# Kernel optimization log

Hardware: AMD Instinct MI355X
Metric: run time of the kernel (lower is better)

The kernel has to match this reference:

```python
import jax, jax.numpy as jnp
import numpy as np

D_MODEL = 1024
H = 16          # n_heads (kv heads)
G = 2           # n_gqa_groups
DQ = 64         # d_queries
DV = 64         # d_values
MAXLEN = 2048
NSEG = 8
SEG = MAXLEN // NSEG  # 256
EPS = 1e-5
ROPE_THETA = 10000.0


def setup_inputs() -> dict:
    key = jax.random.key(0)
    ks = jax.random.split(key, 10)
    N = 8
    w = lambda k, sh: jax.random.normal(k, sh, dtype=jnp.float32) * 0.02
    return {
        "query_sequences": jax.random.normal(ks[0], (N, MAXLEN, D_MODEL), dtype=jnp.float32),
        "key_sequences": jax.random.normal(ks[1], (N, MAXLEN, D_MODEL), dtype=jnp.float32),
        "value_sequences": jax.random.normal(ks[2], (N, MAXLEN, D_MODEL), dtype=jnp.float32),
        "ln_w": jnp.ones((D_MODEL,), dtype=jnp.float32),
        "ln_b": jnp.zeros((D_MODEL,), dtype=jnp.float32),
        "Wq": w(ks[3], (G * H * DQ, D_MODEL)),
        "Wk": w(ks[4], (H * DQ, D_MODEL)),
        "Wv": w(ks[5], (H * DV, D_MODEL)),
        "Wo": w(ks[6], (D_MODEL, H * DV)),
        "Wkc": w(ks[7], (DQ, SEG * DQ)),
        "bkc": jnp.zeros((DQ,), dtype=jnp.float32),
        "Wvc": w(ks[8], (DV, SEG * DV)),
        "bvc": jnp.zeros((DV,), dtype=jnp.float32),
    }


def _layernorm(x, w, b):
    mu = x.mean(-1, keepdims=True)
    var = ((x - mu) ** 2).mean(-1, keepdims=True)
    return (x - mu) * jax.lax.rsqrt(var + EPS) * w + b


def _rope(x):
    # x: [..., seq, DQ]; full-dim interleaved RoPE (rotary-embedding-torch convention)
    seq = x.shape[-2]
    inv_freq = 1.0 / (ROPE_THETA ** (jnp.arange(0, DQ, 2, dtype=jnp.float32) / DQ))  # [DQ/2]
    ang = jnp.arange(seq, dtype=jnp.float32)[:, None] * inv_freq[None, :]            # [seq, DQ/2]
    ang = jnp.repeat(ang, 2, axis=-1)                                                # [seq, DQ]
    cos, sin = jnp.cos(ang), jnp.sin(ang)
    x2 = x.reshape(x.shape[:-1] + (DQ // 2, 2))
    xrot = jnp.stack([-x2[..., 1], x2[..., 0]], axis=-1).reshape(x.shape)
    return x * cos + xrot * sin


def _forward(query_sequences, key_sequences, value_sequences,
             ln_w, ln_b, Wq, Wk, Wv, Wo, Wkc, bkc, Wvc, bvc):
    N, t, _ = query_sequences.shape
    q = _layernorm(query_sequences, ln_w, ln_b)
    k = _layernorm(key_sequences, ln_w, ln_b)
    v = _layernorm(value_sequences, ln_w, ln_b)

    qh = (q @ Wq.T).reshape(N, t, G, H, DQ).transpose(0, 2, 3, 1, 4)  # [N,G,H,t,DQ]
    kh = (k @ Wk.T).reshape(N, t, H, DQ).transpose(0, 2, 1, 3)        # [N,H,T,DQ]
    vh = (v @ Wv.T).reshape(N, t, H, DV).transpose(0, 2, 1, 3)        # [N,H,T,DV]

    qh = _rope(qh)
    kh = _rope(kh)

    # split into NSEG segments along time; keep last 2 raw, compress the rest
    kseg = kh.reshape(N, H, NSEG, SEG, DQ)
    vseg = vh.reshape(N, H, NSEG, SEG, DV)
    recent_k = kseg[:, :, -2:].reshape(N, H, 2 * SEG, DQ)
    recent_v = vseg[:, :, -2:].reshape(N, H, 2 * SEG, DV)
    k_sum = jax.nn.elu(kseg[:, :, :-2].reshape(N, H, NSEG - 2, SEG * DQ) @ Wkc.T + bkc)  # [N,H,S-2,DQ]
    v_sum = jax.nn.elu(vseg[:, :, :-2].reshape(N, H, NSEG - 2, SEG * DV) @ Wvc.T + bvc)
    K = jnp.concatenate([k_sum, recent_k], axis=-2)  # [N,H,Tk,DQ], Tk = (NSEG-2) + 2*SEG
    V = jnp.concatenate([v_sum, recent_v], axis=-2)

    # NOTE: original einsum sums over the GQA group axis g
    attn = jnp.einsum('nghtq,nhTq->nhtT', qh, K) * (1.0 / DQ ** 0.5)
    attn = 30.0 * jnp.tanh(attn / 30.0)  # grok scaled attn

    Tk = K.shape[-2]
    causal = jnp.arange(Tk)[None, :] <= jnp.arange(t)[:, None]  # tril slice [t, Tk]
    attn = jnp.where(causal, attn, -jnp.inf)
    attn = jax.nn.softmax(attn, axis=-1)

    out = jnp.einsum('nhtT,nhTv->nhtv', attn, V)
    out = out.transpose(0, 2, 1, 3).reshape(N, t, H * DV)
    return out @ Wo.T


def reference(query_sequences, key_sequences, value_sequences,
              ln_w, ln_b, Wq, Wk, Wv, Wo, Wkc, bkc, Wvc, bvc):
    return _forward(query_sequences, key_sequences, value_sequences,
                    ln_w, ln_b, Wq, Wk, Wv, Wo, Wkc, bkc, Wvc, bvc)
```

## Files before the change

### kernel.cpp

```cpp
#include <hip/hip_runtime.h>
#include <stdint.h>

#define DEV static __device__ __forceinline__

typedef unsigned short u16;
typedef unsigned int u32;
typedef __attribute__((ext_vector_type(4))) float f32x4;
typedef __attribute__((ext_vector_type(8))) short bf16x8;

DEV float bf2f(u16 u) { u32 x = ((u32)u) << 16; float f; __builtin_memcpy(&f, &x, 4); return f; }
DEV u16 f2bf(float f) { u32 x; __builtin_memcpy(&x, &f, 4); x = x + 0x7fffu + ((x >> 16) & 1u); return (u16)(x >> 16); }
DEV float lo16(u32 p) { u32 x = p << 16; float f; __builtin_memcpy(&f, &x, 4); return f; }
DEV float hi16(u32 p) { u32 x = p & 0xffff0000u; float f; __builtin_memcpy(&f, &x, 4); return f; }
DEV u32 pack2(float a, float b) { return (u32)f2bf(a) | ((u32)f2bf(b) << 16); }

DEV u32 cvtpk(float lo, float hi) {
  u32 r; asm("v_cvt_pk_bf16_f32 %0, %1, %2" : "=v"(r) : "v"(lo), "v"(hi)); return r;
}
DEV bf16x8 pk8(f32x4 a, f32x4 b) {
  union { u32 u[4]; bf16x8 v; } x;
  x.u[0] = cvtpk(a[0], a[1]); x.u[1] = cvtpk(a[2], a[3]);
  x.u[2] = cvtpk(b[0], b[1]); x.u[3] = cvtpk(b[2], b[3]);
  return x.v;
}

DEV f32x4 mfma16(bf16x8 a, bf16x8 b, f32x4 c) {
  return __builtin_amdgcn_mfma_f32_16x16x32_bf16(a, b, c, 0, 0, 0);
}

DEV void gl_lds16(const u16* g, u16* l) {
  __builtin_amdgcn_global_load_lds((const __attribute__((address_space(1))) void*)g,
                                   (__attribute__((address_space(3))) void*)l, 16, 0, 0);
}

__global__ __launch_bounds__(256) void prep_all_kernel(
    const float* __restrict__ Wq, const float* __restrict__ Wk, const float* __restrict__ Wv,
    const float* __restrict__ Wo, const float* __restrict__ Wkc, const float* __restrict__ Wvc,
    u16* __restrict__ wqe, u16* __restrict__ wkb, u16* __restrict__ wvb,
    u16* __restrict__ wob, u16* __restrict__ wkcb, u16* __restrict__ wvcb,
    float* __restrict__ cs) {
  int b = blockIdx.x;
  if (b < 6144) {
    int which = b >> 10;
    int id = (b & 1023) * 256 + threadIdx.x;
    const float* src; u16* dst;
    switch (which) {
      case 0: src = Wq;  dst = wqe;  break;
      case 1: src = Wk;  dst = wkb;  break;
      case 2: src = Wv;  dst = wvb;  break;
      case 3: src = Wo;  dst = wob;  break;
      case 4: src = Wkc; dst = wkcb; break;
      default: src = Wvc; dst = wvcb; break;
    }
    float4 a = ((const float4*)src)[id];
    if (which == 0) {
      float4 c = ((const float4*)Wq)[id + 262144];
      a.x += c.x; a.y += c.y; a.z += c.z; a.w += c.w;
    }
    ushort4 o; o.x = f2bf(a.x); o.y = f2bf(a.y); o.z = f2bf(a.z); o.w = f2bf(a.w);
    ((ushort4*)dst)[id] = o;
  } else {
    int id = (b - 6144) * 256 + threadIdx.x;
    int t = id >> 5, i = id & 31;
    double ang = (double)t * pow(10000.0, -(double)(2 * i) / 64.0);
    cs[id * 2] = (float)cos(ang);
    cs[id * 2 + 1] = (float)sin(ang);
  }
}

__global__ __launch_bounds__(256) void ln_kernel(const float* __restrict__ x, const float* __restrict__ w,
                                                 const float* __restrict__ b, u16* __restrict__ out) {
  int row = blockIdx.x, t = threadIdx.x;
  float4 v = ((const float4*)(x + (size_t)row * 1024))[t];
  float s = v.x + v.y + v.z + v.w;
  float s2 = v.x * v.x + v.y * v.y + v.z * v.z + v.w * v.w;
#pragma unroll
  for (int off = 32; off; off >>= 1) { s += __shfl_xor(s, off, 64); s2 += __shfl_xor(s2, off, 64); }
  __shared__ float red[8];
  if ((t & 63) == 0) { red[t >> 6] = s; red[4 + (t >> 6)] = s2; }
  __syncthreads();
  s = red[0] + red[1] + red[2] + red[3];
  s2 = red[4] + red[5] + red[6] + red[7];
  float mu = s * 0.0009765625f;
  float var = s2 * 0.0009765625f - mu * mu;
  float rstd = rsqrtf(var + 1e-5f);
  float4 wv = ((const float4*)w)[t];
  float4 bv = ((const float4*)b)[t];
  ushort4 o;
  o.x = f2bf((v.x - mu) * rstd * wv.x + bv.x);
  o.y = f2bf((v.y - mu) * rstd * wv.y + bv.y);
  o.z = f2bf((v.z - mu) * rstd * wv.z + bv.z);
  o.w = f2bf((v.w - mu) * rstd * wv.w + bv.w);
  *(ushort4*)(out + (size_t)row * 1024 + t * 4) = o;
}

template <int MODE>
__global__ __launch_bounds__(512, 4) void gemm_nt(const u16* __restrict__ A, const u16* __restrict__ B,
                                                  void* __restrict__ Cout, int M, int Nd, int K,
                                                  const float* __restrict__ cs) {
  __shared__ u16 As[16384], Bs[8192];
  int tid = threadIdx.x, lane = tid & 63, wv = tid >> 6;
  int l15 = lane & 15, lq = lane >> 4;
  int bm = blockIdx.x * 256, bn = blockIdx.y * 128;
  int wm = (wv >> 1) * 64, wn = (wv & 1) * 64;
  int srow_in = lane >> 3, sslot = lane & 7;
  f32x4 acc[4][4] = {};
  for (int k0 = 0; k0 < K; k0 += 64) {
    __syncthreads();
#pragma unroll
    for (int it = 0; it < 4; ++it) {
      int ia = it * 8 + wv;
      int row = ia * 8 + srow_in;
      int gc = sslot ^ (row & 7);
      gl_lds16(A + (size_t)(bm + row) * K + k0 + gc * 8, &As[ia * 512]);
    }
#pragma unroll
    for (int it = 0; it < 2; ++it) {
      int ia = it * 8 + wv;
      int row = ia * 8 + srow_in;
      int gc = sslot ^ (row & 7);
      gl_lds16(B + (size_t)(bn + row) * K + k0 + gc * 8, &Bs[ia * 512]);
    }
    __syncthreads();
#pragma unroll
    for (int h = 0; h < 2; ++h) {
      bf16x8 af[4], bfr[4];
#pragma unroll
      for (int mt = 0; mt < 4; ++mt) {
        int r = wm + mt * 16 + l15;
        af[mt] = *(const bf16x8*)&As[r * 64 + (((h * 4 + lq) ^ (r & 7)) * 8)];
      }
#pragma unroll
      for (int nt = 0; nt < 4; ++nt) {
        int r = wn + nt * 16 + l15;
        bfr[nt] = *(const bf16x8*)&Bs[r * 64 + (((h * 4 + lq) ^ (r & 7)) * 8)];
      }
#pragma unroll
      for (int mt = 0; mt < 4; ++mt)
#pragma unroll
        for (int nt = 0; nt < 4; ++nt)
          acc[mt][nt] = mfma16(af[mt], bfr[nt], acc[mt][nt]);
    }
  }
#pragma unroll
  for (int mt = 0; mt < 4; ++mt)
#pragma unroll
    for (int nt = 0; nt < 4; ++nt)
#pragma unroll
      for (int i = 0; i < 4; ++i) {
        int row = bm + wm + mt * 16 + lq * 4 + i;
        int col = bn + wn + nt * 16 + l15;
        float x = acc[mt][nt][i];
        if (MODE == 1) {
          ((float*)Cout)[(size_t)row * Nd + col] = x;
        } else if (MODE == 0) {
          ((u16*)Cout)[(size_t)row * Nd + col] = f2bf(x);
        } else {
          float xp = __shfl_xor(x, 1, 64);
          int t = row & 2047;
          int i0 = (col & 63) >> 1;
          float2 csv = *(const float2*)(cs + ((size_t)t * 32 + i0) * 2);
          float r = (col & 1) ? (x * csv.x + xp * csv.y) : (x * csv.x - xp * csv.y);
          ((u16*)Cout)[(size_t)row * Nd + col] = f2bf(r);
        }
      }
}

__global__ __launch_bounds__(512) void compress_partial_kernel(
    const u16* __restrict__ kh, const u16* __restrict__ vh,
    const u16* __restrict__ wkcb, const u16* __restrict__ wvcb,
    float* __restrict__ part) {
  int mt = blockIdx.x, ksl = blockIdx.y, kv = blockIdx.z;
  const u16* src = kv ? vh : kh;
  const u16* W = kv ? wvcb : wkcb;
  int tid = threadIdx.x, lane = tid & 63, wv = tid >> 6;
  int l15 = lane & 15, lq = lane >> 4;
  int r = mt * 16 + l15;
  int nh = r / 6, s = r % 6;
  int n = nh >> 4, h = nh & 15;
  const u16* arow = src + ((size_t)(n * 2048 + s * 256)) * 1024 + h * 64;
  f32x4 acc[4] = {};
  int kbase = (ksl * 8 + wv) * 256;
#pragma unroll
  for (int ks = 0; ks < 8; ++ks) {
    int k0 = kbase + ks * 32;
    int tau = k0 >> 6, d0 = k0 & 63;
    bf16x8 a = *(const bf16x8*)(arow + (size_t)tau * 1024 + d0 + lq * 8);
#pragma unroll
    for (int nt = 0; nt < 4; ++nt) {
      bf16x8 b = *(const bf16x8*)(W + (size_t)(nt * 16 + l15) * 16384 + k0 + lq * 8);
      acc[nt] = mfma16(a, b, acc[nt]);
    }
  }
  __shared__ float red[8][16][68];
#pragma unroll
  for (int nt = 0; nt < 4; ++nt)
#pragma unroll
    for (int i = 0; i < 4; ++i)
      red[wv][lq * 4 + i][nt * 16 + l15] = acc[nt][i];
  __syncthreads();
  int row = tid >> 5, o0 = (tid & 31) * 2;
  float v0 = 0.f, v1 = 0.f;
#pragma unroll
  for (int w8 = 0; w8 < 8; ++w8) { v0 += red[w8][row][o0]; v1 += red[w8][row][o0 + 1]; }
  size_t base = ((size_t)(kv * 8 + ksl) * 768 + mt * 16 + row) * 64 + o0;
  part[base] = v0;
  part[base + 1] = v1;
}

__global__ __launch_bounds__(256) void finalize_copy_kernel(
    const float* __restrict__ part, const float* __restrict__ bkc, const float* __restrict__ bvc,
    const u16* __restrict__ kh, const u16* __restrict__ vh,
    u16* __restrict__ kp, u16* __restrict__ vtp) {
  int bid = blockIdx.x;
  if (bid < 2280) {
    int u = bid * 256 + threadIdx.x;
    int dq8 = u & 7; int rest = u >> 3; int Tm6 = rest % 570; int nh = rest / 570;
    if (nh >= 128) return;
    uint4 val = {0, 0, 0, 0};
    if (Tm6 < 512) {
      int n = nh >> 4, h = nh & 15;
      val = *(const uint4*)&kh[((size_t)(n * 2048 + 1536 + Tm6)) * 1024 + h * 64 + dq8 * 8];
    }
    *(uint4*)&kp[((size_t)nh * 576 + 6 + Tm6) * 64 + dq8 * 8] = val;
  } else if (bid < 4584) {
    int u = (bid - 2280) * 256 + threadIdx.x;
    int d = u & 63; int rest = u >> 6; int tch = rest % 72; int nh = rest / 72;
    if (nh >= 128) return;
    int n = nh >> 4, h = nh & 15;
#pragma unroll
    for (int ii = 0; ii < 8; ++ii) {
      int T = tch * 8 + ii;
      if (T < 6) continue;
      u16 v = 0;
      if (T < 518) v = vh[((size_t)(n * 2048 + 1536 + (T - 6))) * 1024 + h * 64 + d];
      vtp[((size_t)nh * 64 + d) * 576 + T] = v;
    }
  } else {
    int b2 = bid - 4584;
    int kv = b2 >= 192;
    int id = (kv ? b2 - 192 : b2) * 256 + threadIdx.x;
    int r = id >> 6, o = id & 63;
    float v = kv ? bvc[o] : bkc[o];
#pragma unroll
    for (int s8 = 0; s8 < 8; ++s8) v += part[((size_t)(kv * 8 + s8) * 768 + r) * 64 + o];
    v = v > 0.f ? v : expm1f(v);
    int nh = r / 6, s = r % 6;
    if (kv) vtp[((size_t)nh * 64 + o) * 576 + s] = f2bf(v);
    else    kp[((size_t)nh * 576 + s) * 64 + o] = f2bf(v);
  }
}

__global__ __launch_bounds__(256) void attn_kernel(const u16* __restrict__ qc, const u16* __restrict__ Kp,
                                                   const u16* __restrict__ VTp, u16* __restrict__ ao) {
  int h = blockIdx.x, qt = blockIdx.y, n = blockIdx.z;
  int tid = threadIdx.x, lane = tid & 63, wv = tid >> 6;
  int l15 = lane & 15, lq = lane >> 4;
  __shared__ u16 KS[4096], VS[4096];
  __shared__ float PS[4][1088];
  int q0 = qt * 64 + wv * 16;
  const u16* qrowp = qc + ((size_t)(n * 2048 + q0 + l15)) * 1024 + h * 64;
  bf16x8 aq0 = *(const bf16x8*)(qrowp + lq * 8);
  bf16x8 aq1 = *(const bf16x8*)(qrowp + 32 + lq * 8);
  const u16* Kph = Kp + (size_t)(n * 16 + h) * 576 * 64;
  const u16* Vph = VTp + (size_t)(n * 16 + h) * 64 * 576;
  f32x4 oa[4] = {};
  float rs[4] = {0.f, 0.f, 0.f, 0.f};
  float* PSW = &PS[wv][0];
  const float C1 = 0.012022458674074693f;
  const float C2 = -86.56170245333781f;
  int nchunks = min(qt + 1, 9);
  int srow0 = tid >> 3, sq0 = tid & 7;
  int srow1 = (256 + tid) >> 3, sq1 = tid & 7;
  int ksw0 = srow0 * 64 + ((sq0 ^ (srow0 & 7)) * 8);
  int ksw1 = srow1 * 64 + ((sq1 ^ (srow1 & 7)) * 8);
  uint4 kr0, kr1, vr0, vr1;
  {
    kr0 = *(const uint4*)&Kph[(size_t)srow0 * 64 + sq0 * 8];
    kr1 = *(const uint4*)&Kph[(size_t)srow1 * 64 + sq1 * 8];
    vr0 = *(const uint4*)&Vph[(size_t)srow0 * 576 + sq0 * 8];
    vr1 = *(const uint4*)&Vph[(size_t)srow1 * 576 + sq1 * 8];
  }
  for (int tc = 0; tc < nchunks; ++tc) {
    __syncthreads();
    *(uint4*)&KS[ksw0] = kr0;
    *(uint4*)&KS[ksw1] = kr1;
    *(uint4*)&VS[ksw0] = vr0;
    *(uint4*)&VS[ksw1] = vr1;
    if (tc + 1 < nchunks) {
      int Tb = (tc + 1) * 64;
      kr0 = *(const uint4*)&Kph[(size_t)(Tb + srow0) * 64 + sq0 * 8];
      kr1 = *(const uint4*)&Kph[(size_t)(Tb + srow1) * 64 + sq1 * 8];
      vr0 = *(const uint4*)&Vph[(size_t)srow0 * 576 + Tb + sq0 * 8];
      vr1 = *(const uint4*)&Vph[(size_t)srow1 * 576 + Tb + sq1 * 8];
    }
    __syncthreads();
    f32x4 sv[4];
    __builtin_amdgcn_s_setprio(1);
#pragma unroll
    for (int tt = 0; tt < 4; ++tt) {
      int row = tt * 16 + l15, r7 = row & 7;
      bf16x8 b0 = *(const bf16x8*)&KS[row * 64 + ((lq ^ r7) * 8)];
      bf16x8 b1 = *(const bf16x8*)&KS[row * 64 + (((4 | lq) ^ r7) * 8)];
      f32x4 c = {0.f, 0.f, 0.f, 0.f};
      c = mfma16(aq0, b0, c);
      c = mfma16(aq1, b1, c);
      sv[tt] = c;
    }
    __builtin_amdgcn_s_setprio(0);
    float p[4][4];
    bool needmask = (tc == qt) || (tc == 8);
    if (needmask) {
      int qb = q0 + lq * 4;
      int Tbase = tc * 64;
#pragma unroll
      for (int tt = 0; tt < 4; ++tt) {
        int T = Tbase + tt * 16 + l15;
        bool tval = (T < 518);
#pragma unroll
        for (int i = 0; i < 4; ++i) {
          float e = __builtin_amdgcn_exp2f(sv[tt][i] * C1);
          float pe = __builtin_amdgcn_exp2f(C2 * __builtin_amdgcn_rcpf(e + 1.f));
          bool ok = tval && (T <= qb + i);
          pe = ok ? pe : 0.f;
          p[tt][i] = pe;
          rs[i] += pe;
        }
      }
    } else {
#pragma unroll
      for (int tt = 0; tt < 4; ++tt)
#pragma unroll
        for (int i = 0; i < 4; ++i) {
          float e = __builtin_amdgcn_exp2f(sv[tt][i] * C1);
          float pe = __builtin_amdgcn_exp2f(C2 * __builtin_amdgcn_rcpf(e + 1.f));
          p[tt][i] = pe;
          rs[i] += pe;
        }
    }
#pragma unroll
    for (int tt = 0; tt < 4; ++tt)
#pragma unroll
      for (int i = 0; i < 4; ++i)
        PSW[(lq * 4 + i) * 68 + tt * 16 + l15] = p[tt][i];
    const float* prow = PSW + l15 * 68;
    f32x4 r0a = *(const f32x4*)(prow + lq * 8);
    f32x4 r0b = *(const f32x4*)(prow + lq * 8 + 4);
    f32x4 r1a = *(const f32x4*)(prow + lq * 8 + 32);
    f32x4 r1b = *(const f32x4*)(prow + lq * 8 + 36);
    bf16x8 pa0 = pk8(r0a, r0b);
    bf16x8 pa1 = pk8(r1a, r1b);
    __builtin_amdgcn_s_setprio(1);
#pragma unroll
    for (int ct = 0; ct < 4; ++ct) {
      int row = ct * 16 + l15, r7 = row & 7;
      bf16x8 bv0 = *(const bf16x8*)&VS[row * 64 + ((lq ^ r7) * 8)];
      bf16x8 bv1 = *(const bf16x8*)&VS[row * 64 + (((4 | lq) ^ r7) * 8)];
      oa[ct] = mfma16(pa0, bv0, oa[ct]);
      oa[ct] = mfma16(pa1, bv1, oa[ct]);
    }
    __builtin_amdgcn_s_setprio(0);
  }
#pragma unroll
  for (int i = 0; i < 4; ++i)
#pragma unroll
    for (int off = 1; off < 16; off <<= 1) rs[i] += __shfl_xor(rs[i], off, 64);
  u16* aop = ao + ((size_t)(n * 2048)) * 1024 + h * 64;
#pragma unroll
  for (int i = 0; i < 4; ++i) {
    float inv = 1.0f / rs[i];
    int q = q0 + lq * 4 + i;
#pragma unroll
    for (int ct = 0; ct < 4; ++ct) {
      int dv = ct * 16 + l15;
      aop[(size_t)q * 1024 + dv] = f2bf(oa[ct][i] * inv);
    }
  }
}

extern "C" void kernel_launch(void* const* d_in, const int* in_sizes, int n_in,
                              void* d_out, int out_size, void* d_ws, size_t ws_size,
                              hipStream_t stream) {
  const float* q_in = (const float*)d_in[0];
  const float* k_in = (const float*)d_in[1];
  const float* v_in = (const float*)d_in[2];
  const float* ln_w = (const float*)d_in[3];
  const float* ln_b = (const float*)d_in[4];
  const float* Wq = (const float*)d_in[5];
  const float* Wk = (const float*)d_in[6];
  const float* Wv = (const float*)d_in[7];
  const float* Wo = (const float*)d_in[8];
  const float* Wkc = (const float*)d_in[9];
  const float* bkc = (const float*)d_in[10];
  const float* Wvc = (const float*)d_in[11];
  const float* bvc = (const float*)d_in[12];

  char* ws = (char*)d_ws;
  const size_t MB = 1u << 20;
  u16* wqe = (u16*)(ws + 0 * MB);
  u16* wkb = (u16*)(ws + 2 * MB);
  u16* wvb = (u16*)(ws + 4 * MB);
  u16* wob = (u16*)(ws + 6 * MB);
  u16* wkcb = (u16*)(ws + 8 * MB);
  u16* wvcb = (u16*)(ws + 10 * MB);
  float* csb = (float*)(ws + 12 * MB);
  u16* xn = (u16*)(ws + 13 * MB);
  float* partf = (float*)(ws + 13 * MB);
  u16* qcb = (u16*)(ws + 45 * MB);
  u16* khb = (u16*)(ws + 77 * MB);
  u16* vhb = (u16*)(ws + 109 * MB);
  u16* kp = (u16*)(ws + 141 * MB);
  u16* vtp = (u16*)(ws + 141 * MB + 9437184);
  u16* aob = khb;

  prep_all_kernel<<<6400, 256, 0, stream>>>(Wq, Wk, Wv, Wo, Wkc, Wvc,
                                            wqe, wkb, wvb, wob, wkcb, wvcb, csb);

  dim3 gg(64, 8);
  ln_kernel<<<16384, 256, 0, stream>>>(q_in, ln_w, ln_b, xn);
  gemm_nt<2><<<gg, 512, 0, stream>>>(xn, wqe, qcb, 16384, 1024, 1024, csb);
  ln_kernel<<<16384, 256, 0, stream>>>(k_in, ln_w, ln_b, xn);
  gemm_nt<2><<<gg, 512, 0, stream>>>(xn, wkb, khb, 16384, 1024, 1024, csb);
  ln_kernel<<<16384, 256, 0, stream>>>(v_in, ln_w, ln_b, xn);
  gemm_nt<0><<<gg, 512, 0, stream>>>(xn, wvb, vhb, 16384, 1024, 1024, csb);

  compress_partial_kernel<<<dim3(48, 8, 2), 512, 0, stream>>>(khb, vhb, wkcb, wvcb, partf);
  finalize_copy_kernel<<<4968, 256, 0, stream>>>(partf, bkc, bvc, khb, vhb, kp, vtp);
  attn_kernel<<<dim3(16, 32, 8), 256, 0, stream>>>(qcb, kp, vtp, aob);
  gemm_nt<1><<<gg, 512, 0, stream>>>(aob, wob, (float*)d_out, 16384, 1024, 1024, csb);
}
```

Before: 391.2 us.

## Fuse three layernorms into one launch and widen attention blocks to 128 queries

The three per-input layernorm launches are merged into a single kernel that writes the Q and K normalized activations into the output buffer as scratch and V into the existing workspace. The attention kernel now uses 512 threads covering 128 query rows per block, so each K/V chunk staged in shared memory is reused by twice as many waves. Waves whose causal range ends early skip compute for later chunks but still take part in the barriers. This cuts launch count and halves K/V staging traffic per query, at the cost of idle waves on partially masked chunks and more shared memory per block.

```diff
diff --git a/kernel.cpp b/kernel.cpp
--- a/kernel.cpp
+++ b/kernel.cpp
@@ -12,7 +12,6 @@
 DEV u16 f2bf(float f) { u32 x; __builtin_memcpy(&x, &f, 4); x = x + 0x7fffu + ((x >> 16) & 1u); return (u16)(x >> 16); }
 DEV float lo16(u32 p) { u32 x = p << 16; float f; __builtin_memcpy(&f, &x, 4); return f; }
 DEV float hi16(u32 p) { u32 x = p & 0xffff0000u; float f; __builtin_memcpy(&f, &x, 4); return f; }
-DEV u32 pack2(float a, float b) { return (u32)f2bf(a) | ((u32)f2bf(b) << 16); }
 
 DEV u32 cvtpk(float lo, float hi) {
   u32 r; asm("v_cvt_pk_bf16_f32 %0, %1, %2" : "=v"(r) : "v"(lo), "v"(hi)); return r;
@@ -68,9 +67,16 @@
   }
 }
 
-__global__ __launch_bounds__(256) void ln_kernel(const float* __restrict__ x, const float* __restrict__ w,
-                                                 const float* __restrict__ b, u16* __restrict__ out) {
-  int row = blockIdx.x, t = threadIdx.x;
+__global__ __launch_bounds__(256) void ln3_kernel(const float* __restrict__ xq, const float* __restrict__ xk,
+                                                  const float* __restrict__ xv,
+                                                  const float* __restrict__ w, const float* __restrict__ b,
+                                                  u16* __restrict__ oq, u16* __restrict__ ok,
+                                                  u16* __restrict__ ov) {
+  int bq = blockIdx.x;
+  int which = bq >> 14, row = bq & 16383;
+  const float* x = which == 0 ? xq : (which == 1 ? xk : xv);
+  u16* out = which == 0 ? oq : (which == 1 ? ok : ov);
+  int t = threadIdx.x;
   float4 v = ((const float4*)(x + (size_t)row * 1024))[t];
   float s = v.x + v.y + v.z + v.w;
   float s2 = v.x * v.x + v.y * v.y + v.z * v.z + v.w * v.w;
@@ -251,14 +257,14 @@
   }
 }
 
-__global__ __launch_bounds__(256) void attn_kernel(const u16* __restrict__ qc, const u16* __restrict__ Kp,
+__global__ __launch_bounds__(512) void attn_kernel(const u16* __restrict__ qc, const u16* __restrict__ Kp,
                                                    const u16* __restrict__ VTp, u16* __restrict__ ao) {
   int h = blockIdx.x, qt = blockIdx.y, n = blockIdx.z;
   int tid = threadIdx.x, lane = tid & 63, wv = tid >> 6;
   int l15 = lane & 15, lq = lane >> 4;
   __shared__ u16 KS[4096], VS[4096];
-  __shared__ float PS[4][1088];
-  int q0 = qt * 64 + wv * 16;
+  __shared__ float PS[8][1088];
+  int q0 = qt * 128 + wv * 16;
   const u16* qrowp = qc + ((size_t)(n * 2048 + q0 + l15)) * 1024 + h * 64;
   bf16x8 aq0 = *(const bf16x8*)(qrowp + lq * 8);
   bf16x8 aq1 = *(const bf16x8*)(qrowp + 32 + lq * 8);
@@ -269,32 +275,26 @@
   float* PSW = &PS[wv][0];
   const float C1 = 0.012022458674074693f;
   const float C2 = -86.56170245333781f;
-  int nchunks = min(qt + 1, 9);
-  int srow0 = tid >> 3, sq0 = tid & 7;
-  int srow1 = (256 + tid) >> 3, sq1 = tid & 7;
-  int ksw0 = srow0 * 64 + ((sq0 ^ (srow0 & 7)) * 8);
-  int ksw1 = srow1 * 64 + ((sq1 ^ (srow1 & 7)) * 8);
-  uint4 kr0, kr1, vr0, vr1;
+  int nchunks = min(2 * qt + 2, 9);
+  int dcw = 2 * qt + (wv >> 2);
+  int srow = tid >> 3, sq = tid & 7;
+  int ksw = srow * 64 + ((sq ^ (srow & 7)) * 8);
+  uint4 kr, vr;
   {
-    kr0 = *(const uint4*)&Kph[(size_t)srow0 * 64 + sq0 * 8];
-    kr1 = *(const uint4*)&Kph[(size_t)srow1 * 64 + sq1 * 8];
-    vr0 = *(const uint4*)&Vph[(size_t)srow0 * 576 + sq0 * 8];
-    vr1 = *(const uint4*)&Vph[(size_t)srow1 * 576 + sq1 * 8];
+    kr = *(const uint4*)&Kph[(size_t)srow * 64 + sq * 8];
+    vr = *(const uint4*)&Vph[(size_t)srow * 576 + sq * 8];
   }
   for (int tc = 0; tc < nchunks; ++tc) {
     __syncthreads();
-    *(uint4*)&KS[ksw0] = kr0;
-    *(uint4*)&KS[ksw1] = kr1;
-    *(uint4*)&VS[ksw0] = vr0;
-    *(uint4*)&VS[ksw1] = vr1;
+    *(uint4*)&KS[ksw] = kr;
+    *(uint4*)&VS[ksw] = vr;
     if (tc + 1 < nchunks) {
       int Tb = (tc + 1) * 64;
-      kr0 = *(const uint4*)&Kph[(size_t)(Tb + srow0) * 64 + sq0 * 8];
-      kr1 = *(const uint4*)&Kph[(size_t)(Tb + srow1) * 64 + sq1 * 8];
-      vr0 = *(const uint4*)&Vph[(size_t)srow0 * 576 + Tb + sq0 * 8];
-      vr1 = *(const uint4*)&Vph[(size_t)srow1 * 576 + Tb + sq1 * 8];
+      kr = *(const uint4*)&Kph[(size_t)(Tb + srow) * 64 + sq * 8];
+      vr = *(const uint4*)&Vph[(size_t)srow * 576 + Tb + sq * 8];
     }
     __syncthreads();
+    if (tc > dcw) continue;
     f32x4 sv[4];
     __builtin_amdgcn_s_setprio(1);
 #pragma unroll
@@ -309,7 +309,7 @@
     }
     __builtin_amdgcn_s_setprio(0);
     float p[4][4];
-    bool needmask = (tc == qt) || (tc == 8);
+    bool needmask = (tc == dcw) || (tc == 8);
     if (needmask) {
       int qb = q0 + lq * 4;
       int Tbase = tc * 64;
@@ -412,20 +412,21 @@
   u16* kp = (u16*)(ws + 141 * MB);
   u16* vtp = (u16*)(ws + 141 * MB + 9437184);
   u16* aob = khb;
+  u16* xq = (u16*)d_out;
+  u16* xk = ((u16*)d_out) + 16777216;
 
   prep_all_kernel<<<6400, 256, 0, stream>>>(Wq, Wk, Wv, Wo, Wkc, Wvc,
                                             wqe, wkb, wvb, wob, wkcb, wvcb, csb);
 
+  ln3_kernel<<<49152, 256, 0, stream>>>(q_in, k_in, v_in, ln_w, ln_b, xq, xk, xn);
+
   dim3 gg(64, 8);
-  ln_kernel<<<16384, 256, 0, stream>>>(q_in, ln_w, ln_b, xn);
-  gemm_nt<2><<<gg, 512, 0, stream>>>(xn, wqe, qcb, 16384, 1024, 1024, csb);
-  ln_kernel<<<16384, 256, 0, stream>>>(k_in, ln_w, ln_b, xn);
-  gemm_nt<2><<<gg, 512, 0, stream>>>(xn, wkb, khb, 16384, 1024, 1024, csb);
-  ln_kernel<<<16384, 256, 0, stream>>>(v_in, ln_w, ln_b, xn);
+  gemm_nt<2><<<gg, 512, 0, stream>>>(xq, wqe, qcb, 16384, 1024, 1024, csb);
+  gemm_nt<2><<<gg, 512, 0, stream>>>(xk, wkb, khb, 16384, 1024, 1024, csb);
   gemm_nt<0><<<gg, 512, 0, stream>>>(xn, wvb, vhb, 16384, 1024, 1024, csb);
 
   compress_partial_kernel<<<dim3(48, 8, 2), 512, 0, stream>>>(khb, vhb, wkcb, wvcb, partf);
   finalize_copy_kernel<<<4968, 256, 0, stream>>>(partf, bkc, bvc, khb, vhb, kp, vtp);
-  attn_kernel<<<dim3(16, 32, 8), 256, 0, stream>>>(qcb, kp, vtp, aob);
+  attn_kernel<<<dim3(16, 16, 8), 512, 0, stream>>>(qcb, kp, vtp, aob);
   gemm_nt<1><<<gg, 512, 0, stream>>>(aob, wob, (float*)d_out, 16384, 1024, 1024, csb);
 }
```

Result: faster. 382.4 us (-2.3%).
